# Optimization experiments

Measured on AMD Instinct MI355X. Metric: run time of the kernel, lower is better.

Reference implementation:

```python
import jax, jax.numpy as jnp
import numpy as np

V = 32000; D = 512; H = 8; DH = D // H; L = 12; E = 8; FF = 2048
B = 2; S = 1024; MAXPOS = 2048
EPS = 1e-6; NEG = -1e9


def _rmsnorm(x, w):
    return x * jax.lax.rsqrt(jnp.mean(x * x, axis=-1, keepdims=True) + EPS) * w


def setup_inputs() -> dict:
    key = jax.random.key(0)
    ks = jax.random.split(key, 10)
    s = 0.02
    n = lambda k, shp: jax.random.normal(k, shp, jnp.float32) * s
    return {
        "input_ids": jax.random.randint(ks[0], (B, S), 0, V),
        "tok_emb": n(ks[1], (V, D)),
        "pos_emb": n(ks[2], (MAXPOS, D)),
        "Wqkv": n(ks[3], (L, D, 3 * D)), "bqkv": jnp.zeros((L, 3 * D), jnp.float32),
        "Wo": n(ks[4], (L, D, D)), "bo": jnp.zeros((L, D), jnp.float32),
        "rW": n(ks[5], (L, D, E)), "rb": jnp.zeros((L, E), jnp.float32),
        "eW1": n(ks[6], (L, E, D, FF)), "eb1": jnp.zeros((L, E, FF), jnp.float32),
        "eW2": n(ks[7], (L, E, FF, D)), "eb2": jnp.zeros((L, E, D), jnp.float32),
        "n1w": jnp.ones((L, D), jnp.float32), "n2w": jnp.ones((L, D), jnp.float32),
        "now": jnp.ones((D,), jnp.float32), "lmW": n(ks[8], (D, V)),
    }


def _forward(input_ids, tok_emb, pos_emb, Wqkv, bqkv, Wo, bo, rW, rb,
             eW1, eb1, eW2, eb2, n1w, n2w, now, lmW):
    x = tok_emb[input_ids] + pos_emb[:S]              # [B,S,D]
    causal = jnp.tril(jnp.ones((S, S), bool))         # lower-triangular mask

    def step(x, p):
        wqkv, bq, wo, bo_, rw, rb_, w1, b1, w2, b2, g1, g2 = p
        # --- causal self-attention ---
        h = _rmsnorm(x, g1)
        qkv = h @ wqkv + bq
        q, k, v = [t.reshape(B, S, H, DH) for t in jnp.split(qkv, 3, axis=-1)]
        scores = jnp.einsum('bqhd,bkhd->bhqk', q, k) / jnp.sqrt(jnp.float32(DH))
        scores = jnp.where(causal, scores, NEG)
        attn = jax.nn.softmax(scores, axis=-1)
        o = jnp.einsum('bhqk,bkhd->bqhd', attn, v).reshape(B, S, D) @ wo + bo_
        x = x + o
        # --- MoE layer, top-1 routing ---
        h = _rmsnorm(x, g2)
        rl = h @ rw + rb_                              # router logits [B,S,E]
        probs = jax.nn.softmax(rl, axis=-1)
        top_w = jnp.max(probs, axis=-1)                # top-1 gate weight [B,S]
        top_i = jnp.argmax(probs, axis=-1)             # expert id [B,S]
        one_hot = jax.nn.one_hot(top_i, E, dtype=x.dtype)
        frac = jnp.mean(one_hot, axis=(0, 1))          # fraction of tokens per expert
        pmean = jnp.mean(probs, axis=(0, 1))           # mean router prob per expert
        aux = E * jnp.sum(frac * pmean)                # switch-style load-balance loss
        disp = (one_hot * top_w[..., None]).reshape(-1, E)   # [T,E] weighted dispatch
        hf = h.reshape(-1, D)                          # [T,D]
        hid = jax.nn.gelu(jnp.einsum('td,edf->etf', hf, w1) + b1[:, None, :], approximate=False)
        outs = jnp.einsum('etf,efd->etd', hid, w2) + b2[:, None, :]
        y = jnp.einsum('etd,te->td', outs, disp).reshape(B, S, D)  # scatter-combine
        x = x + y
        return x, (aux, rl)

    x, (auxes, rlogits) = jax.lax.scan(
        step, x, (Wqkv, bqkv, Wo, bo, rW, rb, eW1, eb1, eW2, eb2, n1w, n2w))
    logits = _rmsnorm(x, now) @ lmW                    # [B,S,V]
    return logits, jnp.sum(auxes), rlogits


def reference(input_ids, tok_emb, pos_emb, Wqkv, bqkv, Wo, bo, rW, rb,
              eW1, eb1, eW2, eb2, n1w, n2w, now, lmW):
    return _forward(input_ids, tok_emb, pos_emb, Wqkv, bqkv, Wo, bo, rW, rb,
                    eW1, eb1, eW2, eb2, n1w, n2w, now, lmW)
```

## Files before the change

### kernel.cpp

```cpp
#include <hip/hip_runtime.h>

constexpr int B_  = 2, S_ = 1024, T_ = 2048;
constexpr int D_  = 512, H_ = 8, DH_ = 64;
constexpr int L_  = 12, E_ = 8, FF_ = 2048;
constexpr int V_  = 32000, D3_ = 1536;

using half8_t = __attribute__((ext_vector_type(8))) _Float16;
using half2_t = __attribute__((ext_vector_type(2))) _Float16;
using f32x4_t = __attribute__((ext_vector_type(4))) float;

__device__ __forceinline__ float wred(float v){
#pragma unroll
  for (int off = 32; off; off >>= 1) v += __shfl_xor(v, off);
  return v;
}
__device__ __forceinline__ float gelu_f(float v){
  return 0.5f * v * (1.f + erff(v * 0.70710678118654752f));
}

__global__ void k_embed(const int* __restrict__ ids, const float* __restrict__ tok,
                        const float* __restrict__ pos, float* __restrict__ x){
  int t = blockIdx.x;
  int s = t & (S_ - 1);
  int id = ids[t];
  const float* tr = tok + (size_t)id * D_;
  const float* pr = pos + (size_t)s  * D_;
  float* xr = x + (size_t)t * D_;
  for (int d = threadIdx.x; d < D_; d += blockDim.x) xr[d] = tr[d] + pr[d];
}

__global__ __launch_bounds__(64) void k_norm_router(
    const float* __restrict__ x, const float* __restrict__ nw,
    const float* __restrict__ rW, const float* __restrict__ rb,
    float* __restrict__ h, float* __restrict__ rl_out,
    float* __restrict__ topw, int* __restrict__ topi){
  const int t = blockIdx.x, lane = threadIdx.x;
  const float* xr = x + (size_t)t * D_;
  const float4 xv0 = *reinterpret_cast<const float4*>(xr + (lane << 2));
  const float4 xv1 = *reinterpret_cast<const float4*>(xr + 256 + (lane << 2));
  float ss = xv0.x*xv0.x + xv0.y*xv0.y + xv0.z*xv0.z + xv0.w*xv0.w
           + xv1.x*xv1.x + xv1.y*xv1.y + xv1.z*xv1.z + xv1.w*xv1.w;
  ss = wred(ss);
  const float sc = rsqrtf(ss * (1.f / (float)D_) + 1e-6f);
  const float4 w0 = *reinterpret_cast<const float4*>(nw + (lane << 2));
  const float4 w1 = *reinterpret_cast<const float4*>(nw + 256 + (lane << 2));
  float hv[8];
  hv[0] = xv0.x*sc*w0.x; hv[1] = xv0.y*sc*w0.y; hv[2] = xv0.z*sc*w0.z; hv[3] = xv0.w*sc*w0.w;
  hv[4] = xv1.x*sc*w1.x; hv[5] = xv1.y*sc*w1.y; hv[6] = xv1.z*sc*w1.z; hv[7] = xv1.w*sc*w1.w;
  float* hr = h + (size_t)t * D_;
  *reinterpret_cast<float4*>(hr + (lane << 2))       = make_float4(hv[0], hv[1], hv[2], hv[3]);
  *reinterpret_cast<float4*>(hr + 256 + (lane << 2)) = make_float4(hv[4], hv[5], hv[6], hv[7]);
  float acc[8] = {0,0,0,0,0,0,0,0};
#pragma unroll
  for (int u = 0; u < 8; u++){
    const int d = (u < 4) ? ((lane << 2) + u) : (256 + (lane << 2) + u - 4);
    const float4 ra = *reinterpret_cast<const float4*>(rW + (size_t)d * E_);
    const float4 rb4 = *reinterpret_cast<const float4*>(rW + (size_t)d * E_ + 4);
    acc[0] += hv[u]*ra.x;  acc[1] += hv[u]*ra.y;  acc[2] += hv[u]*ra.z;  acc[3] += hv[u]*ra.w;
    acc[4] += hv[u]*rb4.x; acc[5] += hv[u]*rb4.y; acc[6] += hv[u]*rb4.z; acc[7] += hv[u]*rb4.w;
  }
  float rl[8];
#pragma unroll
  for (int e = 0; e < 8; e++) rl[e] = wred(acc[e]) + rb[e];
  float mx = rl[0];
#pragma unroll
  for (int e = 1; e < 8; e++) mx = fmaxf(mx, rl[e]);
  float p[8], s = 0.f;
#pragma unroll
  for (int e = 0; e < 8; e++){ p[e] = __expf(rl[e] - mx); s += p[e]; }
  const float inv = 1.f / s;
  int arg = 0; float best = rl[0];
#pragma unroll
  for (int e = 1; e < 8; e++) if (rl[e] > best){ best = rl[e]; arg = e; }
  if (lane == 0){
#pragma unroll
    for (int e = 0; e < 8; e++) rl_out[(size_t)t * E_ + e] = rl[e];
    topw[t] = p[arg] * inv;
    topi[t] = arg;
  }
}

__global__ __launch_bounds__(1024) void k_route_scan2(
    const int* __restrict__ topi, const float* __restrict__ rl,
    int* __restrict__ seg, int* __restrict__ perm, float* __restrict__ aux){
  __shared__ int cnt[8], segs[9], cur[8];
  __shared__ float psums[8];
  const int tid = threadIdx.x;
  if (tid < 8){ cnt[tid] = 0; psums[tid] = 0.f; }
  __syncthreads();
  const int t0 = tid, t1 = tid + 1024;
  const int e0 = topi[t0], e1 = topi[t1];
  atomicAdd(&cnt[e0], 1);
  atomicAdd(&cnt[e1], 1);
  float ps[8] = {0,0,0,0,0,0,0,0};
#pragma unroll
  for (int k = 0; k < 2; k++){
    const float* r = rl + (size_t)(k ? t1 : t0) * E_;
    float v[8];
#pragma unroll
    for (int e = 0; e < 8; e++) v[e] = r[e];
    float mx = v[0];
#pragma unroll
    for (int e = 1; e < 8; e++) mx = fmaxf(mx, v[e]);
    float s = 0.f;
#pragma unroll
    for (int e = 0; e < 8; e++){ v[e] = __expf(v[e] - mx); s += v[e]; }
    const float is = 1.f / s;
#pragma unroll
    for (int e = 0; e < 8; e++) ps[e] += v[e] * is;
  }
#pragma unroll
  for (int e = 0; e < 8; e++) ps[e] = wred(ps[e]);
  if ((tid & 63) == 0){
#pragma unroll
    for (int e = 0; e < 8; e++) atomicAdd(&psums[e], ps[e]);
  }
  __syncthreads();
  if (tid == 0){
    segs[0] = 0;
#pragma unroll
    for (int e = 0; e < 8; e++) segs[e + 1] = segs[e] + cnt[e];
#pragma unroll
    for (int e = 0; e < 8; e++) cur[e] = segs[e];
  }
  __syncthreads();
  if (tid < 9) seg[tid] = segs[tid];
  const int p0 = atomicAdd(&cur[e0], 1); perm[p0] = t0;
  const int p1 = atomicAdd(&cur[e1], 1); perm[p1] = t1;
  if (tid == 0){
    float av = 0.f;
#pragma unroll
    for (int e = 0; e < 8; e++) av += (float)cnt[e] * psums[e];
    aux[0] += 8.f * av * (1.f / ((float)T_ * (float)T_));
  }
}

__global__ __launch_bounds__(256) void k_prep_lm(const float* __restrict__ Bsrc,
                                                 _Float16* __restrict__ Bpre){
  const int gid = blockIdx.x * 256 + threadIdx.x;
  const int n = gid % V_;
  const int kb = gid / V_;
  const int kstep = kb >> 3, kgl = kb & 7;
  const int ks2 = kgl >> 2, kg = kgl & 3;
  const int colTile = n >> 7, nl = n & 127;
  const int sub = nl >> 4;
  const int lsw = ((nl & 15) + (kg << 4)) ^ (sub & 7);
  half8_t v;
#pragma unroll
  for (int e = 0; e < 8; e++) v[e] = (_Float16)Bsrc[(size_t)(kb * 8 + e) * V_ + n];
  *reinterpret_cast<half8_t*>(
      &Bpre[((size_t)(colTile * 8 + kstep) << 13) + ks2 * 4096 + sub * 512 + lsw * 8]) = v;
}

template<int BM, int BN, int NPROD, int EPI, bool MOE, bool APERM, int SWZROWS, bool ANORM, bool BPRE>
__global__ __launch_bounds__(256) void k_mgemm(
    const float* __restrict__ A, const float* __restrict__ Bm,
    const float* __restrict__ bias, float* __restrict__ C,
    int M, int N, int K,
    const int* __restrict__ seg, const int* __restrict__ perm,
    const float* __restrict__ topw, const float* __restrict__ nw,
    const _Float16* __restrict__ Bpre){
  constexpr int FM = BM / 32, FN = BN / 32;
  constexpr int AKS = BM * 32, BKS = BN * 32;
  constexpr int BSLOTS = BN / 32;
  const int tid = threadIdx.x;
  int rowTile, colTile;
  if (SWZROWS > 0){
    const int nwg = gridDim.x;
    const int bid = blockIdx.x;
    const int lb = (bid & 7) * (nwg >> 3) + (bid >> 3);
    rowTile = lb % SWZROWS;
    colTile = lb / SWZROWS;
  } else {
    colTile = blockIdx.x; rowTile = blockIdx.y;
  }
  int e = 0, s0 = 0, cnt = M;
  if (MOE){ e = blockIdx.z; s0 = seg[e]; cnt = seg[e + 1] - s0; }
  const int row0 = rowTile * BM, col0 = colTile * BN;
  if (MOE && row0 >= cnt) return;
  const float* Bp = Bm + (size_t)e * K * N;
  const float* bp = bias + (size_t)e * N;

  __shared__ __align__(16) _Float16 Ah[BM * 64];
  __shared__ __align__(16) _Float16 Al[NPROD == 3 ? BM * 64 : 8];
  __shared__ __align__(16) _Float16 Bh[BN * 64];
  __shared__ __align__(16) _Float16 Bl[NPROD == 3 ? BN * 64 : 8];

  const int am = (BM == 64) ? (tid >> 2) : (tid >> 1);
  const int agrow = row0 + am;
  const bool aval = agrow < cnt;
  const float* Arow = nullptr;
  if (aval){
    int ridx = APERM ? perm[s0 + agrow] : (MOE ? s0 + agrow : agrow);
    Arow = A + (size_t)ridx * K;
  }
  const int asub = am >> 4;

  const int lane = tid & 63, w = tid >> 6;
  const int wm0 = (w >> 1) * (BM / 2), wn0 = (w & 1) * (BN / 2);

  float ascale = 1.f;
  if (ANORM){
    float ss = 0.f;
    if (BM == 64){
      const int kg = tid & 3;
      for (int k0 = 0; k0 < K; k0 += 32){
        const float4 a0 = *reinterpret_cast<const float4*>(Arow + k0 + (kg << 3));
        const float4 a1 = *reinterpret_cast<const float4*>(Arow + k0 + (kg << 3) + 4);
        ss += a0.x*a0.x + a0.y*a0.y + a0.z*a0.z + a0.w*a0.w
            + a1.x*a1.x + a1.y*a1.y + a1.z*a1.z + a1.w*a1.w;
      }
      ss += __shfl_xor(ss, 1);
      ss += __shfl_xor(ss, 2);
    } else {
      const int kgb = (tid & 1) << 1;
      for (int k0 = 0; k0 < K; k0 += 32){
#pragma unroll
        for (int kq = 0; kq < 2; kq++){
          const int kg = kgb + kq;
          const float4 a0 = *reinterpret_cast<const float4*>(Arow + k0 + (kg << 3));
          const float4 a1 = *reinterpret_cast<const float4*>(Arow + k0 + (kg << 3) + 4);
          ss += a0.x*a0.x + a0.y*a0.y + a0.z*a0.z + a0.w*a0.w
              + a1.x*a1.x + a1.y*a1.y + a1.z*a1.z + a1.w*a1.w;
        }
      }
      ss += __shfl_xor(ss, 1);
    }
    ascale = rsqrtf(ss * (1.f / (float)K) + 1e-6f);
  }

  f32x4_t acc_hh[FM][FN];
  f32x4_t acc_mx[NPROD == 3 ? FM : 1][NPROD == 3 ? FN : 1];
#pragma unroll
  for (int i = 0; i < FM; i++)
#pragma unroll
    for (int j = 0; j < FN; j++){
      acc_hh[i][j] = (f32x4_t){0.f, 0.f, 0.f, 0.f};
      if (NPROD == 3) acc_mx[i][j] = (f32x4_t){0.f, 0.f, 0.f, 0.f};
    }

  for (int k0 = 0; k0 < K; k0 += 64){
    {
      constexpr int NCH = (BM == 64) ? 2 : 4;
      const int kq = (BM == 64) ? (tid & 3) : (tid & 1);
#pragma unroll
      for (int c = 0; c < NCH; c++){
        const int kgt = kq * NCH + c;
        const int k = k0 + (kgt << 3);
        float4 a0 = make_float4(0,0,0,0), a1 = make_float4(0,0,0,0);
        if (aval){
          a0 = *reinterpret_cast<const float4*>(Arow + k);
          a1 = *reinterpret_cast<const float4*>(Arow + k + 4);
        }
        float a8[8] = {a0.x, a0.y, a0.z, a0.w, a1.x, a1.y, a1.z, a1.w};
        if (ANORM){
          const float4 w0 = *reinterpret_cast<const float4*>(nw + k);
          const float4 w1 = *reinterpret_cast<const float4*>(nw + k + 4);
          const float wn8[8] = {w0.x, w0.y, w0.z, w0.w, w1.x, w1.y, w1.z, w1.w};
#pragma unroll
          for (int u = 0; u < 8; u++) a8[u] *= ascale * wn8[u];
        }
        half8_t hi, lo;
#pragma unroll
        for (int u = 0; u < 8; u++){
          hi[u] = (_Float16)a8[u];
          if (NPROD == 3) lo[u] = (_Float16)((a8[u] - (float)hi[u]) * 2048.f);
        }
        const int ks2 = kgt >> 2, kg = kgt & 3;
        const int lidx = (am & 15) + (kg << 4);
        const int base = ks2 * AKS + asub * 512 + ((lidx ^ (asub & 7)) << 3);
        *reinterpret_cast<half8_t*>(&Ah[base]) = hi;
        if (NPROD == 3) *reinterpret_cast<half8_t*>(&Al[base]) = lo;
      }
    }
    if (BPRE){
      const _Float16* bsrc = Bpre + (((size_t)colTile * (K >> 6) + (k0 >> 6)) << 13);
#pragma unroll
      for (int r = 0; r < 4; r++){
        const int ofs = (r * 256 + tid) * 8;
        *reinterpret_cast<half8_t*>(&Bh[ofs]) =
            *reinterpret_cast<const half8_t*>(&bsrc[ofs]);
      }
    } else {
#pragma unroll
      for (int sl = 0; sl < BSLOTS; sl++){
        const int sid = sl * 256 + tid;
        const int col = sid & (BN - 1);
        const int kgt = sid / BN;
        const float* bpp = Bp + (size_t)(k0 + (kgt << 3)) * N + col0 + col;
        half8_t hi, lo;
#pragma unroll
        for (int ee = 0; ee < 8; ee++){
          const float v = bpp[(size_t)ee * N];
          hi[ee] = (_Float16)v;
          if (NPROD == 3) lo[ee] = (_Float16)((v - (float)hi[ee]) * 2048.f);
        }
        const int ks2 = kgt >> 2, kg = kgt & 3;
        const int sub = col >> 4;
        const int lidx = (col & 15) + (kg << 4);
        const int base = ks2 * BKS + sub * 512 + ((lidx ^ (sub & 7)) << 3);
        *reinterpret_cast<half8_t*>(&Bh[base]) = hi;
        if (NPROD == 3) *reinterpret_cast<half8_t*>(&Bl[base]) = lo;
      }
    }
    __syncthreads();
#pragma unroll
    for (int ks2 = 0; ks2 < 2; ks2++){
      half8_t fAh[FM], fBh[FN];
      half8_t fAl[NPROD == 3 ? FM : 1], fBl[NPROD == 3 ? FN : 1];
#pragma unroll
      for (int fm = 0; fm < FM; fm++){
        const int s = (wm0 >> 4) + fm;
        const int ofs = ks2 * AKS + s * 512 + ((lane ^ (s & 7)) << 3);
        fAh[fm] = *reinterpret_cast<const half8_t*>(&Ah[ofs]);
        if (NPROD == 3) fAl[fm] = *reinterpret_cast<const half8_t*>(&Al[ofs]);
      }
#pragma unroll
      for (int fn = 0; fn < FN; fn++){
        const int s = (wn0 >> 4) + fn;
        const int ofs = ks2 * BKS + s * 512 + ((lane ^ (s & 7)) << 3);
        fBh[fn] = *reinterpret_cast<const half8_t*>(&Bh[ofs]);
        if (NPROD == 3) fBl[fn] = *reinterpret_cast<const half8_t*>(&Bl[ofs]);
      }
#pragma unroll
      for (int fm = 0; fm < FM; fm++)
#pragma unroll
        for (int fn = 0; fn < FN; fn++){
          acc_hh[fm][fn] = __builtin_amdgcn_mfma_f32_16x16x32_f16(
              fAh[fm], fBh[fn], acc_hh[fm][fn], 0, 0, 0);
          if (NPROD == 3){
            acc_mx[fm][fn] = __builtin_amdgcn_mfma_f32_16x16x32_f16(
                fAh[fm], fBl[fn], acc_mx[fm][fn], 0, 0, 0);
            acc_mx[fm][fn] = __builtin_amdgcn_mfma_f32_16x16x32_f16(
                fAl[fm], fBh[fn], acc_mx[fm][fn], 0, 0, 0);
          }
        }
    }
    __syncthreads();
  }

  const int lr = lane & 15, kg4 = lane >> 4;
#pragma unroll
  for (int fm = 0; fm < FM; fm++){
#pragma unroll
    for (int reg = 0; reg < 4; reg++){
      const int grow = row0 + wm0 + fm * 16 + (kg4 << 2) + reg;
      if (grow >= cnt) continue;
      int trow = 0; float tw = 0.f;
      if (EPI == 3){ trow = perm[s0 + grow]; tw = topw[trow]; }
#pragma unroll
      for (int fn = 0; fn < FN; fn++){
        const int col = col0 + wn0 + fn * 16 + lr;
        float v = acc_hh[fm][fn][reg];
        if (NPROD == 3) v += acc_mx[fm][fn][reg] * (1.f / 2048.f);
        if (EPI == 0){
          C[(size_t)grow * N + col] = v + bp[col];
        } else if (EPI == 1){
          C[(size_t)grow * N + col] += v + bp[col];
        } else if (EPI == 2){
          C[(size_t)(s0 + grow) * N + col] = gelu_f(v + bp[col]);
        } else if (EPI == 3){
          C[(size_t)trow * N + col] += tw * (v + bp[col]);
        } else {
          C[(size_t)grow * N + col] = v;
        }
      }
    }
  }
}

__global__ __launch_bounds__(256) void k_attn5(const float* __restrict__ qkv,
                                               float* __restrict__ o,
                                               float* __restrict__ attp,
                                               float* __restrict__ attml){
  __shared__ __align__(16) _Float16 Khi[4096], Klo[4096], Vhi[4096], Vlo[4096];
  __shared__ __align__(16) float pbuf[4][16 * 68];
  const int tid = threadIdx.x, w = tid >> 6, lane = tid & 63;
  const int lr = lane & 15, g = lane >> 4;
  const int bid = blockIdx.x;
  int bh, qt, kt0, kt1, mode;
  if (bid < 128){        bh = bid >> 3;            qt = 8 + (bid & 7);  kt0 = 0; kt1 = 7;  mode = 1; }
  else if (bid < 256){   const int j = bid - 128;  bh = j >> 3; qt = 7 - (j & 7);  kt0 = 0; kt1 = qt; mode = 0; }
  else {                 const int j = bid - 256;  bh = j >> 3; qt = 15 - (j & 7); kt0 = 8; kt1 = qt; mode = 2; }
  const int b = bh >> 3, h = bh & 7;
  const size_t bbase = (size_t)(b << 10) * D3_;
  const int hoff = h * 64;
  const int qg = (qt << 6) + (w << 4) + lr;

  half8_t qhi[2], qlo[2];
#pragma unroll
  for (int ks = 0; ks < 2; ks++){
    const float* qp = qkv + bbase + (size_t)qg * D3_ + hoff + ks * 32 + g * 8;
    const float4 f0 = *reinterpret_cast<const float4*>(qp);
    const float4 f1 = *reinterpret_cast<const float4*>(qp + 4);
    const float qa[8] = {f0.x, f0.y, f0.z, f0.w, f1.x, f1.y, f1.z, f1.w};
#pragma unroll
    for (int e = 0; e < 8; e++){
      const float v = qa[e] * 0.125f;
      const _Float16 hi = (_Float16)v;
      qhi[ks][e] = hi;
      qlo[ks][e] = (_Float16)((v - (float)hi) * 2048.f);
    }
  }

  float m = -1e30f, l = 0.f;
  f32x4_t oacc[4];
#pragma unroll
  for (int s = 0; s < 4; s++) oacc[s] = (f32x4_t){0.f, 0.f, 0.f, 0.f};

  const int kK = tid >> 2, quad = tid & 3;
  const int kp = tid >> 3, oct = tid & 7;

  float ka[16], va[8], vb[8];
  auto loadregs = [&](int kt){
    const int j0 = kt << 6;
    const float* kr = qkv + bbase + (size_t)(j0 + kK) * D3_ + 512 + hoff + quad * 16;
    const float4 f0 = *reinterpret_cast<const float4*>(kr);
    const float4 f1 = *reinterpret_cast<const float4*>(kr + 4);
    const float4 f2 = *reinterpret_cast<const float4*>(kr + 8);
    const float4 f3 = *reinterpret_cast<const float4*>(kr + 12);
    ka[0]=f0.x; ka[1]=f0.y; ka[2]=f0.z; ka[3]=f0.w;
    ka[4]=f1.x; ka[5]=f1.y; ka[6]=f1.z; ka[7]=f1.w;
    ka[8]=f2.x; ka[9]=f2.y; ka[10]=f2.z; ka[11]=f2.w;
    ka[12]=f3.x; ka[13]=f3.y; ka[14]=f3.z; ka[15]=f3.w;
    const int k0v = kp << 1;
    const float* vr = qkv + bbase + (size_t)(j0 + k0v) * D3_ + 1024 + hoff + oct * 8;
    const float4 a0 = *reinterpret_cast<const float4*>(vr);
    const float4 a1 = *reinterpret_cast<const float4*>(vr + 4);
    const float4 b0 = *reinterpret_cast<const float4*>(vr + D3_);
    const float4 b1 = *reinterpret_cast<const float4*>(vr + D3_ + 4);
    va[0]=a0.x; va[1]=a0.y; va[2]=a0.z; va[3]=a0.w;
    va[4]=a1.x; va[5]=a1.y; va[6]=a1.z; va[7]=a1.w;
    vb[0]=b0.x; vb[1]=b0.y; vb[2]=b0.z; vb[3]=b0.w;
    vb[4]=b1.x; vb[5]=b1.y; vb[6]=b1.z; vb[7]=b1.w;
  };
  auto writelds = [&](){
    const int ksd = quad >> 1;
#pragma unroll
    for (int ch = 0; ch < 2; ch++){
      const int kgd = ((quad << 1) + ch) & 3;
      const int base = ksd * 2048 + (kK >> 4) * 512 + (((kK & 15) + (kgd << 4)) << 3);
      half8_t hi, lo;
#pragma unroll
      for (int e = 0; e < 8; e++){
        const float v = ka[ch * 8 + e];
        const _Float16 hv = (_Float16)v;
        hi[e] = hv;
        lo[e] = (_Float16)((v - (float)hv) * 2048.f);
      }
      *reinterpret_cast<half8_t*>(&Khi[base]) = hi;
      *reinterpret_cast<half8_t*>(&Klo[base]) = lo;
    }
    const int ksk = kp >> 4, kgk = (kp >> 2) & 3, e0 = (kp & 3) << 1;
#pragma unroll
    for (int j = 0; j < 8; j++){
      const int d = oct * 8 + j;
      const int lidx = (d & 15) + (kgk << 4);
      const int sw = lidx ^ kgk ^ (ksk << 2);
      const int fa = ksk * 2048 + (d >> 4) * 512 + (sw << 3) + e0;
      const _Float16 h0 = (_Float16)va[j], h1 = (_Float16)vb[j];
      *reinterpret_cast<half2_t*>(&Vhi[fa]) = (half2_t){h0, h1};
      const _Float16 l0 = (_Float16)((va[j] - (float)h0) * 2048.f);
      const _Float16 l1 = (_Float16)((vb[j] - (float)h1) * 2048.f);
      *reinterpret_cast<half2_t*>(&Vlo[fa]) = (half2_t){l0, l1};
    }
  };

  loadregs(kt0);
  for (int kt = kt0; kt <= kt1; kt++){
    const int j0 = kt << 6;
    __syncthreads();
    writelds();
    if (kt < kt1) loadregs(kt + 1);
    __syncthreads();

    f32x4_t dfr[4];
#pragma unroll
    for (int s = 0; s < 4; s++){
      f32x4_t acc = (f32x4_t){0.f, 0.f, 0.f, 0.f};
      f32x4_t mix = (f32x4_t){0.f, 0.f, 0.f, 0.f};
#pragma unroll
      for (int ks = 0; ks < 2; ks++){
        const int base = ks * 2048 + s * 512 + lane * 8;
        const half8_t khi = *reinterpret_cast<const half8_t*>(&Khi[base]);
        const half8_t klo = *reinterpret_cast<const half8_t*>(&Klo[base]);
        acc = __builtin_amdgcn_mfma_f32_16x16x32_f16(khi, qhi[ks], acc, 0, 0, 0);
        mix = __builtin_amdgcn_mfma_f32_16x16x32_f16(khi, qlo[ks], mix, 0, 0, 0);
        mix = __builtin_amdgcn_mfma_f32_16x16x32_f16(klo, qhi[ks], mix, 0, 0, 0);
      }
#pragma unroll
      for (int r = 0; r < 4; r++) dfr[s][r] = acc[r] + mix[r] * (1.f / 2048.f);
    }
    if (kt == qt){
#pragma unroll
      for (int s = 0; s < 4; s++)
#pragma unroll
        for (int r = 0; r < 4; r++){
          const int keyg = j0 + (g << 2) + r + (s << 4);
          if (keyg > qg) dfr[s][r] = -1e30f;
        }
    }
    float mloc = dfr[0][0];
#pragma unroll
    for (int s = 0; s < 4; s++)
#pragma unroll
      for (int r = 0; r < 4; r++) mloc = fmaxf(mloc, dfr[s][r]);
    mloc = fmaxf(mloc, __shfl_xor(mloc, 16));
    mloc = fmaxf(mloc, __shfl_xor(mloc, 32));
    const float mn = fmaxf(m, mloc);
    const float cr = __expf(m - mn);
    float psum = 0.f;
#pragma unroll
    for (int s = 0; s < 4; s++)
#pragma unroll
      for (int r = 0; r < 4; r++){
        const float p = __expf(dfr[s][r] - mn);
        psum += p;
        pbuf[w][lr * 68 + (s << 4) + (g << 2) + r] = p;
      }
    psum += __shfl_xor(psum, 16);
    psum += __shfl_xor(psum, 32);
    l = l * cr + psum;
    m = mn;
#pragma unroll
    for (int s = 0; s < 4; s++)
#pragma unroll
      for (int r = 0; r < 4; r++) oacc[s][r] *= cr;

    half8_t phi[2], plo[2];
#pragma unroll
    for (int ks = 0; ks < 2; ks++){
      const float* pp = &pbuf[w][lr * 68 + ks * 32 + g * 8];
      const float4 p0 = *reinterpret_cast<const float4*>(pp);
      const float4 p1 = *reinterpret_cast<const float4*>(pp + 4);
      const float pa[8] = {p0.x,p0.y,p0.z,p0.w, p1.x,p1.y,p1.z,p1.w};
#pragma unroll
      for (int e = 0; e < 8; e++){
        const _Float16 hv = (_Float16)pa[e];
        phi[ks][e] = hv;
        plo[ks][e] = (_Float16)((pa[e] - (float)hv) * 2048.f);
      }
    }
#pragma unroll
    for (int s = 0; s < 4; s++){
      f32x4_t mix = (f32x4_t){0.f, 0.f, 0.f, 0.f};
#pragma unroll
      for (int ks = 0; ks < 2; ks++){
        const int sw = lane ^ g ^ (ks << 2);
        const int base = ks * 2048 + s * 512 + sw * 8;
        const half8_t vhi = *reinterpret_cast<const half8_t*>(&Vhi[base]);
        const half8_t vlo = *reinterpret_cast<const half8_t*>(&Vlo[base]);
        oacc[s] = __builtin_amdgcn_mfma_f32_16x16x32_f16(vhi, phi[ks], oacc[s], 0, 0, 0);
        mix = __builtin_amdgcn_mfma_f32_16x16x32_f16(vhi, plo[ks], mix, 0, 0, 0);
        mix = __builtin_amdgcn_mfma_f32_16x16x32_f16(vlo, phi[ks], mix, 0, 0, 0);
      }
#pragma unroll
      for (int r = 0; r < 4; r++) oacc[s][r] += mix[r] * (1.f / 2048.f);
    }
  }

  if (mode == 0){
    const float linv = 1.f / l;
    float* orow = o + (size_t)((b << 10) + qg) * D_ + hoff;
#pragma unroll
    for (int s = 0; s < 4; s++)
#pragma unroll
      for (int r = 0; r < 4; r++){
        const int d = (g << 2) + r + (s << 4);
        orow[d] = oacc[s][r] * linv;
      }
  } else {
    const int pidx = (((bh << 3) + (qt - 8)) << 1) + (mode - 1);
    float* pO = attp + (size_t)pidx * 4096;
    const int qloc = (w << 4) + lr;
#pragma unroll
    for (int s = 0; s < 4; s++)
#pragma unroll
      for (int r = 0; r < 4; r++){
        const int d = (g << 2) + r + (s << 4);
        pO[qloc * 64 + d] = oacc[s][r];
      }
    if (g == 0){
      attml[pidx * 128 + qloc]      = m;
      attml[pidx * 128 + 64 + qloc] = l;
    }
  }
}

__global__ __launch_bounds__(256) void k_attn_comb(const float* __restrict__ attp,
                                                   const float* __restrict__ attml,
                                                   float* __restrict__ o){
  const int bid = blockIdx.x;
  const int bh = bid >> 3, i = bid & 7, qt = 8 + i;
  const int b = bh >> 3, h = bh & 7;
  const int pidx0 = ((bh << 3) + i) << 1;
  const float* pA = attp + (size_t)pidx0 * 4096;
  const float* pB = pA + 4096;
  const float* mlA = attml + pidx0 * 128;
  const float* mlB = mlA + 128;
  const int tid = threadIdx.x;
  const int q = tid >> 2, dg = (tid & 3) << 4;
  const float mA = mlA[q], lA = mlA[64 + q];
  const float mB = mlB[q], lB = mlB[64 + q];
  const float M = fmaxf(mA, mB);
  const float cA = __expf(mA - M), cB = __expf(mB - M);
  const float linv = 1.f / (lA * cA + lB * cB);
  float* orow = o + (size_t)((b << 10) + (qt << 6) + q) * D_ + h * 64;
#pragma unroll
  for (int j = 0; j < 4; j++){
    const int d = dg + (j << 2);
    const float4 a = *reinterpret_cast<const float4*>(pA + q * 64 + d);
    const float4 bb = *reinterpret_cast<const float4*>(pB + q * 64 + d);
    *reinterpret_cast<float4*>(orow + d) = make_float4(
        (a.x * cA + bb.x * cB) * linv, (a.y * cA + bb.y * cB) * linv,
        (a.z * cA + bb.z * cB) * linv, (a.w * cA + bb.w * cB) * linv);
  }
}

extern "C" void kernel_launch(void* const* d_in, const int* in_sizes, int n_in,
                              void* d_out, int out_size, void* d_ws, size_t ws_size,
                              hipStream_t stream){
  const int*   ids  = (const int*)  d_in[0];
  const float* tok  = (const float*)d_in[1];
  const float* pos  = (const float*)d_in[2];
  const float* Wqkv = (const float*)d_in[3];
  const float* bqkv = (const float*)d_in[4];
  const float* Wo   = (const float*)d_in[5];
  const float* bo   = (const float*)d_in[6];
  const float* rW   = (const float*)d_in[7];
  const float* rb   = (const float*)d_in[8];
  const float* eW1  = (const float*)d_in[9];
  const float* eb1  = (const float*)d_in[10];
  const float* eW2  = (const float*)d_in[11];
  const float* eb2  = (const float*)d_in[12];
  const float* n1w  = (const float*)d_in[13];
  const float* n2w  = (const float*)d_in[14];
  const float* noww = (const float*)d_in[15];
  const float* lmW  = (const float*)d_in[16];

  float* out    = (float*)d_out;
  float* logits = out;
  float* aux    = out + (size_t)T_ * V_;
  float* rlog   = aux + 1;

  float* ws = (float*)d_ws;
  size_t off = 0;
  float* x     = ws + off; off += (size_t)T_ * D_;
  float* h     = ws + off; off += (size_t)T_ * D_;
  float* qkv   = ws + off; off += (size_t)T_ * D3_;
  float* attno = ws + off; off += (size_t)T_ * D_;
  float* hid   = ws + off; off += (size_t)T_ * FF_;
  float* topw  = ws + off; off += T_;
  int* topi    = (int*)(ws + off); off += T_;
  int* perm    = (int*)(ws + off); off += T_;
  int* seg     = (int*)(ws + off); off += (E_ + 1);
  float* attp  = ws + off; off += 16 * 8 * 2 * 4096;
  float* attml = ws + off; off += 16 * 8 * 2 * 128;

  hipMemsetAsync(aux, 0, sizeof(float), stream);
  k_embed<<<T_, 256, 0, stream>>>(ids, tok, pos, x);

  for (int l = 0; l < L_; l++){
    k_mgemm<64, 128, 3, 0, false, false, 0, true, false><<<dim3(D3_ / 128, T_ / 64), 256, 0, stream>>>(
        x, Wqkv + (size_t)l * D_ * D3_, bqkv + (size_t)l * D3_, qkv,
        T_, D3_, D_, seg, perm, topw, n1w + (size_t)l * D_, nullptr);
    k_attn5<<<384, 256, 0, stream>>>(qkv, attno, attp, attml);
    k_attn_comb<<<128, 256, 0, stream>>>(attp, attml, attno);
    k_mgemm<64, 64, 3, 1, false, false, 0, false, false><<<dim3(D_ / 64, T_ / 64), 256, 0, stream>>>(
        attno, Wo + (size_t)l * D_ * D_, bo + (size_t)l * D_, x,
        T_, D_, D_, seg, perm, topw, nullptr, nullptr);
    k_norm_router<<<T_, 64, 0, stream>>>(x, n2w + (size_t)l * D_,
        rW + (size_t)l * D_ * E_, rb + (size_t)l * E_,
        h, rlog + (size_t)l * T_ * E_, topw, topi);
    k_route_scan2<<<1, 1024, 0, stream>>>(topi, rlog + (size_t)l * T_ * E_, seg, perm, aux);
    k_mgemm<64, 128, 3, 2, true, true, 0, false, false><<<dim3(FF_ / 128, T_ / 64, E_), 256, 0, stream>>>(
        h, eW1 + (size_t)l * E_ * D_ * FF_, eb1 + (size_t)l * E_ * FF_, hid,
        T_, FF_, D_, seg, perm, topw, nullptr, nullptr);
    k_mgemm<64, 64, 3, 3, true, false, 0, false, false><<<dim3(D_ / 64, T_ / 64, E_), 256, 0, stream>>>(
        hid, eW2 + (size_t)l * E_ * FF_ * D_, eb2 + (size_t)l * E_ * D_, x,
        T_, D_, FF_, seg, perm, topw, nullptr, nullptr);
  }

  _Float16* lmw16 = (_Float16*)qkv;
  k_prep_lm<<<(64 * V_) / 256, 256, 0, stream>>>(lmW, lmw16);
  k_mgemm<128, 128, 1, 4, false, false, 16, true, true><<<(T_ / 128) * (V_ / 128), 256, 0, stream>>>(
      x, lmW, nullptr, logits, T_, V_, D_, seg, perm, topw, noww, lmw16);
}
```

Baseline: 3.197 ms.

## Fuse attention combine and routing scan into producers via last-block atomics

```diff
diff --git a/kernel.cpp b/kernel.cpp
--- a/kernel.cpp
+++ b/kernel.cpp
@@ -29,73 +29,82 @@
   for (int d = threadIdx.x; d < D_; d += blockDim.x) xr[d] = tr[d] + pr[d];
 }
 
-__global__ __launch_bounds__(64) void k_norm_router(
+__global__ __launch_bounds__(256) void k_norm_router2(
     const float* __restrict__ x, const float* __restrict__ nw,
     const float* __restrict__ rW, const float* __restrict__ rb,
     float* __restrict__ h, float* __restrict__ rl_out,
-    float* __restrict__ topw, int* __restrict__ topi){
-  const int t = blockIdx.x, lane = threadIdx.x;
-  const float* xr = x + (size_t)t * D_;
-  const float4 xv0 = *reinterpret_cast<const float4*>(xr + (lane << 2));
-  const float4 xv1 = *reinterpret_cast<const float4*>(xr + 256 + (lane << 2));
-  float ss = xv0.x*xv0.x + xv0.y*xv0.y + xv0.z*xv0.z + xv0.w*xv0.w
-           + xv1.x*xv1.x + xv1.y*xv1.y + xv1.z*xv1.z + xv1.w*xv1.w;
-  ss = wred(ss);
-  const float sc = rsqrtf(ss * (1.f / (float)D_) + 1e-6f);
-  const float4 w0 = *reinterpret_cast<const float4*>(nw + (lane << 2));
-  const float4 w1 = *reinterpret_cast<const float4*>(nw + 256 + (lane << 2));
-  float hv[8];
-  hv[0] = xv0.x*sc*w0.x; hv[1] = xv0.y*sc*w0.y; hv[2] = xv0.z*sc*w0.z; hv[3] = xv0.w*sc*w0.w;
-  hv[4] = xv1.x*sc*w1.x; hv[5] = xv1.y*sc*w1.y; hv[6] = xv1.z*sc*w1.z; hv[7] = xv1.w*sc*w1.w;
-  float* hr = h + (size_t)t * D_;
-  *reinterpret_cast<float4*>(hr + (lane << 2))       = make_float4(hv[0], hv[1], hv[2], hv[3]);
-  *reinterpret_cast<float4*>(hr + 256 + (lane << 2)) = make_float4(hv[4], hv[5], hv[6], hv[7]);
-  float acc[8] = {0,0,0,0,0,0,0,0};
-#pragma unroll
-  for (int u = 0; u < 8; u++){
-    const int d = (u < 4) ? ((lane << 2) + u) : (256 + (lane << 2) + u - 4);
-    const float4 ra = *reinterpret_cast<const float4*>(rW + (size_t)d * E_);
-    const float4 rb4 = *reinterpret_cast<const float4*>(rW + (size_t)d * E_ + 4);
-    acc[0] += hv[u]*ra.x;  acc[1] += hv[u]*ra.y;  acc[2] += hv[u]*ra.z;  acc[3] += hv[u]*ra.w;
-    acc[4] += hv[u]*rb4.x; acc[5] += hv[u]*rb4.y; acc[6] += hv[u]*rb4.z; acc[7] += hv[u]*rb4.w;
-  }
-  float rl[8];
-#pragma unroll
-  for (int e = 0; e < 8; e++) rl[e] = wred(acc[e]) + rb[e];
-  float mx = rl[0];
-#pragma unroll
-  for (int e = 1; e < 8; e++) mx = fmaxf(mx, rl[e]);
-  float p[8], s = 0.f;
-#pragma unroll
-  for (int e = 0; e < 8; e++){ p[e] = __expf(rl[e] - mx); s += p[e]; }
-  const float inv = 1.f / s;
-  int arg = 0; float best = rl[0];
-#pragma unroll
-  for (int e = 1; e < 8; e++) if (rl[e] > best){ best = rl[e]; arg = e; }
-  if (lane == 0){
-#pragma unroll
-    for (int e = 0; e < 8; e++) rl_out[(size_t)t * E_ + e] = rl[e];
-    topw[t] = p[arg] * inv;
-    topi[t] = arg;
-  }
-}
-
-__global__ __launch_bounds__(1024) void k_route_scan2(
-    const int* __restrict__ topi, const float* __restrict__ rl,
-    int* __restrict__ seg, int* __restrict__ perm, float* __restrict__ aux){
+    float* __restrict__ topw, int* __restrict__ topi,
+    int* __restrict__ done, int* __restrict__ seg,
+    int* __restrict__ perm, float* __restrict__ aux){
+  const int tid = threadIdx.x, wv = tid >> 6, lane = tid & 63;
+  const int t = (blockIdx.x << 2) + wv;
+  {
+    const float* xr = x + (size_t)t * D_;
+    const float4 xv0 = *reinterpret_cast<const float4*>(xr + (lane << 2));
+    const float4 xv1 = *reinterpret_cast<const float4*>(xr + 256 + (lane << 2));
+    float ss = xv0.x*xv0.x + xv0.y*xv0.y + xv0.z*xv0.z + xv0.w*xv0.w
+             + xv1.x*xv1.x + xv1.y*xv1.y + xv1.z*xv1.z + xv1.w*xv1.w;
+    ss = wred(ss);
+    const float sc = rsqrtf(ss * (1.f / (float)D_) + 1e-6f);
+    const float4 w0 = *reinterpret_cast<const float4*>(nw + (lane << 2));
+    const float4 w1 = *reinterpret_cast<const float4*>(nw + 256 + (lane << 2));
+    float hv[8];
+    hv[0] = xv0.x*sc*w0.x; hv[1] = xv0.y*sc*w0.y; hv[2] = xv0.z*sc*w0.z; hv[3] = xv0.w*sc*w0.w;
+    hv[4] = xv1.x*sc*w1.x; hv[5] = xv1.y*sc*w1.y; hv[6] = xv1.z*sc*w1.z; hv[7] = xv1.w*sc*w1.w;
+    float* hr = h + (size_t)t * D_;
+    *reinterpret_cast<float4*>(hr + (lane << 2))       = make_float4(hv[0], hv[1], hv[2], hv[3]);
+    *reinterpret_cast<float4*>(hr + 256 + (lane << 2)) = make_float4(hv[4], hv[5], hv[6], hv[7]);
+    float acc[8] = {0,0,0,0,0,0,0,0};
+#pragma unroll
+    for (int u = 0; u < 8; u++){
+      const int d = (u < 4) ? ((lane << 2) + u) : (256 + (lane << 2) + u - 4);
+      const float4 ra = *reinterpret_cast<const float4*>(rW + (size_t)d * E_);
+      const float4 rb4 = *reinterpret_cast<const float4*>(rW + (size_t)d * E_ + 4);
+      acc[0] += hv[u]*ra.x;  acc[1] += hv[u]*ra.y;  acc[2] += hv[u]*ra.z;  acc[3] += hv[u]*ra.w;
+      acc[4] += hv[u]*rb4.x; acc[5] += hv[u]*rb4.y; acc[6] += hv[u]*rb4.z; acc[7] += hv[u]*rb4.w;
+    }
+    float rl[8];
+#pragma unroll
+    for (int e = 0; e < 8; e++) rl[e] = wred(acc[e]) + rb[e];
+    float mx = rl[0];
+#pragma unroll
+    for (int e = 1; e < 8; e++) mx = fmaxf(mx, rl[e]);
+    float p[8], s = 0.f;
+#pragma unroll
+    for (int e = 0; e < 8; e++){ p[e] = __expf(rl[e] - mx); s += p[e]; }
+    const float inv = 1.f / s;
+    int arg = 0; float best = rl[0];
+#pragma unroll
+    for (int e = 1; e < 8; e++) if (rl[e] > best){ best = rl[e]; arg = e; }
+    if (lane == 0){
+#pragma unroll
+      for (int e = 0; e < 8; e++) rl_out[(size_t)t * E_ + e] = rl[e];
+      topw[t] = p[arg] * inv;
+      topi[t] = arg;
+    }
+  }
+  __threadfence();
+  __syncthreads();
+  __shared__ int lastFlag;
+  if (tid == 0) lastFlag = atomicAdd(done, 1);
+  __syncthreads();
+  if (lastFlag != 511) return;
+  __threadfence();
   __shared__ int cnt[8], segs[9], cur[8];
   __shared__ float psums[8];
-  const int tid = threadIdx.x;
   if (tid < 8){ cnt[tid] = 0; psums[tid] = 0.f; }
   __syncthreads();
-  const int t0 = tid, t1 = tid + 1024;
-  const int e0 = topi[t0], e1 = topi[t1];
-  atomicAdd(&cnt[e0], 1);
-  atomicAdd(&cnt[e1], 1);
+  const int tb = tid << 3;
+  int myE[8];
+#pragma unroll
+  for (int i = 0; i < 8; i++){
+    myE[i] = topi[tb + i];
+    atomicAdd(&cnt[myE[i]], 1);
+  }
   float ps[8] = {0,0,0,0,0,0,0,0};
 #pragma unroll
-  for (int k = 0; k < 2; k++){
-    const float* r = rl + (size_t)(k ? t1 : t0) * E_;
+  for (int i = 0; i < 8; i++){
+    const float* r = rl_out + (size_t)(tb + i) * E_;
     float v[8];
 #pragma unroll
     for (int e = 0; e < 8; e++) v[e] = r[e];
@@ -111,7 +120,7 @@
   }
 #pragma unroll
   for (int e = 0; e < 8; e++) ps[e] = wred(ps[e]);
-  if ((tid & 63) == 0){
+  if (lane == 0){
 #pragma unroll
     for (int e = 0; e < 8; e++) atomicAdd(&psums[e], ps[e]);
   }
@@ -125,8 +134,11 @@
   }
   __syncthreads();
   if (tid < 9) seg[tid] = segs[tid];
-  const int p0 = atomicAdd(&cur[e0], 1); perm[p0] = t0;
-  const int p1 = atomicAdd(&cur[e1], 1); perm[p1] = t1;
+#pragma unroll
+  for (int i = 0; i < 8; i++){
+    const int p = atomicAdd(&cur[myE[i]], 1);
+    perm[p] = tb + i;
+  }
   if (tid == 0){
     float av = 0.f;
 #pragma unroll
@@ -372,7 +384,8 @@
 __global__ __launch_bounds__(256) void k_attn5(const float* __restrict__ qkv,
                                                float* __restrict__ o,
                                                float* __restrict__ attp,
-                                               float* __restrict__ attml){
+                                               float* __restrict__ attml,
+                                               int* __restrict__ paircnt){
   __shared__ __align__(16) _Float16 Khi[4096], Klo[4096], Vhi[4096], Vlo[4096];
   __shared__ __align__(16) float pbuf[4][16 * 68];
   const int tid = threadIdx.x, w = tid >> 6, lane = tid & 63;
@@ -570,7 +583,8 @@
         orow[d] = oacc[s][r] * linv;
       }
   } else {
-    const int pidx = (((bh << 3) + (qt - 8)) << 1) + (mode - 1);
+    const int pairi = (bh << 3) + (qt - 8);
+    const int pidx = (pairi << 1) + (mode - 1);
     float* pO = attp + (size_t)pidx * 4096;
     const int qloc = (w << 4) + lr;
 #pragma unroll
@@ -584,36 +598,37 @@
       attml[pidx * 128 + qloc]      = m;
       attml[pidx * 128 + 64 + qloc] = l;
     }
-  }
-}
-
-__global__ __launch_bounds__(256) void k_attn_comb(const float* __restrict__ attp,
-                                                   const float* __restrict__ attml,
-                                                   float* __restrict__ o){
-  const int bid = blockIdx.x;
-  const int bh = bid >> 3, i = bid & 7, qt = 8 + i;
-  const int b = bh >> 3, h = bh & 7;
-  const int pidx0 = ((bh << 3) + i) << 1;
-  const float* pA = attp + (size_t)pidx0 * 4096;
-  const float* pB = pA + 4096;
-  const float* mlA = attml + pidx0 * 128;
-  const float* mlB = mlA + 128;
-  const int tid = threadIdx.x;
-  const int q = tid >> 2, dg = (tid & 3) << 4;
-  const float mA = mlA[q], lA = mlA[64 + q];
-  const float mB = mlB[q], lB = mlB[64 + q];
-  const float M = fmaxf(mA, mB);
-  const float cA = __expf(mA - M), cB = __expf(mB - M);
-  const float linv = 1.f / (lA * cA + lB * cB);
-  float* orow = o + (size_t)((b << 10) + (qt << 6) + q) * D_ + h * 64;
-#pragma unroll
-  for (int j = 0; j < 4; j++){
-    const int d = dg + (j << 2);
-    const float4 a = *reinterpret_cast<const float4*>(pA + q * 64 + d);
-    const float4 bb = *reinterpret_cast<const float4*>(pB + q * 64 + d);
-    *reinterpret_cast<float4*>(orow + d) = make_float4(
-        (a.x * cA + bb.x * cB) * linv, (a.y * cA + bb.y * cB) * linv,
-        (a.z * cA + bb.z * cB) * linv, (a.w * cA + bb.w * cB) * linv);
+    __threadfence();
+    __syncthreads();
+    __shared__ int lastFlag;
+    if (tid == 0) lastFlag = atomicAdd(&paircnt[pairi], 1);
+    __syncthreads();
+    if (lastFlag == 1){
+      __threadfence();
+      const int pidx0 = pairi << 1;
+      const float* pA = attp + (size_t)pidx0 * 4096;
+      const float* pB = pA + 4096;
+      const float* mlA = attml + pidx0 * 128;
+      const float* mlB = mlA + 128;
+      const int q = tid >> 2, dg = (tid & 3) << 4;
+      const float mA = mlA[q], lA = mlA[64 + q];
+      const float mB = mlB[q], lB = mlB[64 + q];
+      const float M = fmaxf(mA, mB);
+      const float cA = __expf(mA - M), cB = __expf(mB - M);
+      const float linv = 1.f / (lA * cA + lB * cB);
+      float* orow = o + (size_t)((b << 10) + (qt << 6 & ~4095) + ((qt & 15) << 6) + q) * D_;
+      const int qtp = 8 + (pairi & 7);
+      orow = o + (size_t)((b << 10) + (qtp << 6) + q) * D_ + h * 64;
+#pragma unroll
+      for (int j = 0; j < 4; j++){
+        const int d = dg + (j << 2);
+        const float4 a = *reinterpret_cast<const float4*>(pA + q * 64 + d);
+        const float4 bb = *reinterpret_cast<const float4*>(pB + q * 64 + d);
+        *reinterpret_cast<float4*>(orow + d) = make_float4(
+            (a.x * cA + bb.x * cB) * linv, (a.y * cA + bb.y * cB) * linv,
+            (a.z * cA + bb.z * cB) * linv, (a.w * cA + bb.w * cB) * linv);
+      }
+    }
   }
 }
 
@@ -656,23 +671,25 @@
   int* seg     = (int*)(ws + off); off += (E_ + 1);
   float* attp  = ws + off; off += 16 * 8 * 2 * 4096;
   float* attml = ws + off; off += 16 * 8 * 2 * 128;
-
+  int* synccnt = (int*)(ws + off); off += 12 * 136;
+
+  hipMemsetAsync(synccnt, 0, 12 * 136 * sizeof(int), stream);
   hipMemsetAsync(aux, 0, sizeof(float), stream);
   k_embed<<<T_, 256, 0, stream>>>(ids, tok, pos, x);
 
   for (int l = 0; l < L_; l++){
+    int* lcnt = synccnt + l * 136;
     k_mgemm<64, 128, 3, 0, false, false, 0, true, false><<<dim3(D3_ / 128, T_ / 64), 256, 0, stream>>>(
         x, Wqkv + (size_t)l * D_ * D3_, bqkv + (size_t)l * D3_, qkv,
         T_, D3_, D_, seg, perm, topw, n1w + (size_t)l * D_, nullptr);
-    k_attn5<<<384, 256, 0, stream>>>(qkv, attno, attp, attml);
-    k_attn_comb<<<128, 256, 0, stream>>>(attp, attml, attno);
+    k_attn5<<<384, 256, 0, stream>>>(qkv, attno, attp, attml, lcnt);
     k_mgemm<64, 64, 3, 1, false, false, 0, false, false><<<dim3(D_ / 64, T_ / 64), 256, 0, stream>>>(
         attno, Wo + (size_t)l * D_ * D_, bo + (size_t)l * D_, x,
         T_, D_, D_, seg, perm, topw, nullptr, nullptr);
-    k_norm_router<<<T_, 64, 0, stream>>>(x, n2w + (size_t)l * D_,
+    k_norm_router2<<<T_ / 4, 256, 0, stream>>>(x, n2w + (size_t)l * D_,
         rW + (size_t)l * D_ * E_, rb + (size_t)l * E_,
-        h, rlog + (size_t)l * T_ * E_, topw, topi);
-    k_route_scan2<<<1, 1024, 0, stream>>>(topi, rlog + (size_t)l * T_ * E_, seg, perm, aux);
+        h, rlog + (size_t)l * T_ * E_, topw, topi,
+        lcnt + 128, seg, perm, aux);
     k_mgemm<64, 128, 3, 2, true, true, 0, false, false><<<dim3(FF_ / 128, T_ / 64, E_), 256, 0, stream>>>(
         h, eW1 + (size_t)l * E_ * D_ * FF_, eb1 + (size_t)l * E_ * FF_, hid,
         T_, FF_, D_, seg, perm, topw, nullptr, nullptr);
```

Result: slower. 4.265 ms (+33.4%).
